# Optimization experiments

Measured on AMD Instinct MI355X. Metric: run time of the kernel, lower is better.

The kernel has to match this reference:

```python
import jax, jax.numpy as jnp
import numpy as np

IN_DIMS = 4
DEPTH = 4
C = IN_DIMS + 1                     # channels after time augmentation
SIG = sum(C ** k for k in range(1, DEPTH + 1))  # 780
N, T = 64, 1024


def setup_inputs() -> dict:
    key = jax.random.key(0)
    k1, k2, k3, k4, k5 = jax.random.split(key, 5)
    batch = jax.random.normal(k1, (N, T, IN_DIMS), dtype=jnp.float32)
    s_c = 1.0 / np.sqrt(C)
    conv_w = jax.random.normal(k2, (C, C), dtype=jnp.float32) * s_c
    conv_b = jax.random.normal(k3, (C,), dtype=jnp.float32) * s_c
    s_l = 1.0 / np.sqrt(SIG)
    lin_w = jax.random.normal(k4, (SIG, SIG), dtype=jnp.float32) * s_l
    lin_b = jax.random.normal(k5, (SIG,), dtype=jnp.float32) * s_l
    return {"batch": batch, "conv_w": conv_w, "conv_b": conv_b,
            "lin_w": lin_w, "lin_b": lin_b}


def _stream_signature(path):
    """Streamed path signature with zero basepoint.

    path: (n, t, C). Returns (n, t, SIG) where entry t is the signature of
    the piecewise-linear path (0, path[0], ..., path[t]) truncated at DEPTH,
    levels flattened in lexicographic (row-major) order like signatory.
    """
    n = path.shape[0]
    # increments; basepoint=True means first increment is path[:,0] - 0
    dx = jnp.concatenate([path[:, :1, :], path[:, 1:, :] - path[:, :-1, :]], axis=1)
    init = tuple(jnp.zeros((n, C ** k), path.dtype) for k in range(1, DEPTH + 1))

    def step(levels, d):
        # exp(d) in the truncated tensor algebra: e_k = d^{(x)k} / k!
        e = [d]
        for k in range(2, DEPTH + 1):
            e.append((jnp.einsum('na,nb->nab', e[-1], d) / k).reshape(n, -1))
        # Chen: new_k = e_k + S_k + sum_{i=1}^{k-1} S_i (x) e_{k-i}
        new = []
        for k in range(1, DEPTH + 1):
            acc = levels[k - 1] + e[k - 1]
            for i in range(1, k):
                acc = acc + jnp.einsum('na,nb->nab', levels[i - 1], e[k - i - 1]).reshape(n, -1)
            new.append(acc)
        new = tuple(new)
        return new, jnp.concatenate(new, axis=-1)

    _, ys = jax.lax.scan(step, init, jnp.swapaxes(dx, 0, 1))  # ys: (t, n, SIG)
    return jnp.swapaxes(ys, 0, 1)


def reference(batch, conv_w, conv_b, lin_w, lin_b):
    n, t, _ = batch.shape
    # time augmentation: append channel arange(1,T+1)/T
    time = (jnp.arange(1, t + 1, dtype=batch.dtype) / t)[None, :, None]
    a = jnp.concatenate([batch, jnp.broadcast_to(time, (n, t, 1))], axis=-1)  # (n,t,C)
    # kernel-size-1 conv1d == pointwise linear over channels
    b = a @ conv_w.T + conv_b                                                  # (n,t,C)
    c = _stream_signature(b)                                                   # (n,t,SIG)
    # zero out the first stream entry (torch.concat of zeros with c[:,1:,:])
    c = jnp.concatenate([jnp.zeros((n, 1, SIG), c.dtype), c[:, 1:, :]], axis=1)
    return jnp.tanh(c @ lin_w.T + lin_b)
```

## Files before the change

### kernel.cpp

```cpp
#include <hip/hip_runtime.h>
#include <math.h>

#define N_B 64
#define T_LEN 1024
#define IN_D 4
#define CH 5
#define SIG 780
#define KP 800
#define SEG_LEN 16
#define N_SEG 64
#define SC_L1 1.0f
#define SC_L2 0.25f
#define SC_L3 0.0625f
#define SC_L4 0.015625f

typedef _Float16 f16x8 __attribute__((ext_vector_type(8)));
typedef float f32x4 __attribute__((ext_vector_type(4)));

typedef __attribute__((address_space(1))) const void* as1cp;
typedef __attribute__((address_space(3))) void* as3p;

#define VMCNT(n) asm volatile("s_waitcnt vmcnt(" #n ")" ::: "memory")

__device__ __forceinline__ float fast_tanh(float x) {
  float ax = fabsf(x);
  float e = __expf(-2.0f * ax);
  float r = (1.0f - e) * __builtin_amdgcn_rcpf(1.0f + e);
  return copysignf(r, x);
}

__global__ __launch_bounds__(256) void conv_kernel(
    const float* __restrict__ batch,
    const float* __restrict__ conv_w,
    const float* __restrict__ conv_b,
    float* __restrict__ b_out) {
  int idx = blockIdx.x * blockDim.x + threadIdx.x;
  if (idx >= N_B * T_LEN) return;
  int t = idx & (T_LEN - 1);
  const float* a = batch + (size_t)idx * IN_D;
  float a0 = a[0], a1 = a[1], a2 = a[2], a3 = a[3];
  float tm = (float)(t + 1) / (float)T_LEN;
  float* o = b_out + (size_t)idx * CH;
#pragma unroll
  for (int j = 0; j < CH; ++j) {
    const float* w = conv_w + j * CH;
    float r = conv_b[j];
    r = fmaf(tm, w[4], r);
    r = fmaf(a3, w[3], r);
    r = fmaf(a2, w[2], r);
    r = fmaf(a1, w[1], r);
    r = fmaf(a0, w[0], r);
    o[j] = r;
  }
}

__global__ __launch_bounds__(320) void seg_kernel(
    const float* __restrict__ batch,
    const float* __restrict__ conv_w,
    const float* __restrict__ conv_b,
    float* __restrict__ P) {
  int s = blockIdx.x;
  int n = blockIdx.y;
  int tid = threadIdx.x;

  __shared__ float S[2][SIG];
  __shared__ float bc[(SEG_LEN + 1) * CH];
  __shared__ float dsh[SEG_LEN][CH];

  for (int i = tid; i < SIG; i += 320) S[0][i] = 0.0f;
  if (tid < (SEG_LEN + 1) * CH) {
    int r = s * SEG_LEN - 1 + tid / CH, ch = tid % CH;
    float v = 0.0f;
    if (r >= 0) {
      const float* a = batch + ((size_t)n * T_LEN + r) * IN_D;
      const float* w = conv_w + ch * CH;
      v = conv_b[ch];
      v = fmaf(a[0], w[0], v);
      v = fmaf(a[1], w[1], v);
      v = fmaf(a[2], w[2], v);
      v = fmaf(a[3], w[3], v);
      v = fmaf((float)(r + 1) * (1.0f / T_LEN), w[4], v);
    }
    bc[tid] = v;
  }
  __syncthreads();
  if (tid < SEG_LEN * CH) {
    int j = tid / CH, ch = tid % CH;
    dsh[j][ch] = bc[(j + 1) * CH + ch] - bc[j * CH + ch];
  }

  const int x0 = tid;
  const int x1 = tid + 320;
  const bool has1 = (tid < 305);
  const int a0i = x0 / 125, b0i = (x0 / 25) % 5, c0i = (x0 / 5) % 5, d0i = x0 % 5;
  const int a1i = x1 / 125, b1i = (x1 / 25) % 5, c1i = (x1 / 5) % 5, d1i = x1 % 5;
  const int s2_0 = x0 / 25, s3_0 = x0 / 5;
  const int s2_1 = x1 / 25, s3_1 = x1 / 5;
  const bool hasL3 = (tid < 125);
  const int ya = tid / 25, yb = (tid / 5) % 5, yc = tid % 5;
  const bool hasL2 = (tid < 25);
  const int za = tid / 5, zb = tid % 5;
  const bool hasL1 = (tid < CH);
  __syncthreads();

  int c = 0;
  for (int j = 0; j < SEG_LEN; ++j) {
    const float* Sc = S[c];
    float* Sn = S[c ^ 1];
    float n4_0, n4_1 = 0.0f, n3 = 0.0f, n2 = 0.0f, n1 = 0.0f;
    {
      float tH = fmaf(0.25f, dsh[j][a0i], Sc[a0i]);
      tH = fmaf((1.0f / 3.0f) * dsh[j][b0i], tH, Sc[5 + s2_0]);
      tH = fmaf(0.5f * dsh[j][c0i], tH, Sc[30 + s3_0]);
      n4_0 = fmaf(dsh[j][d0i], tH, Sc[155 + x0]);
    }
    if (has1) {
      float tH = fmaf(0.25f, dsh[j][a1i], Sc[a1i]);
      tH = fmaf((1.0f / 3.0f) * dsh[j][b1i], tH, Sc[5 + s2_1]);
      tH = fmaf(0.5f * dsh[j][c1i], tH, Sc[30 + s3_1]);
      n4_1 = fmaf(dsh[j][d1i], tH, Sc[155 + x1]);
    }
    if (hasL3) {
      float tH = fmaf((1.0f / 3.0f), dsh[j][ya], Sc[ya]);
      tH = fmaf(0.5f * dsh[j][yb], tH, Sc[5 + ya * 5 + yb]);
      n3 = fmaf(dsh[j][yc], tH, Sc[30 + tid]);
    }
    if (hasL2) {
      float tH = fmaf(0.5f, dsh[j][za], Sc[za]);
      n2 = fmaf(dsh[j][zb], tH, Sc[5 + tid]);
    }
    if (hasL1) n1 = Sc[tid] + dsh[j][tid];
    Sn[155 + x0] = n4_0;
    if (has1) Sn[155 + x1] = n4_1;
    if (hasL3) Sn[30 + tid] = n3;
    if (hasL2) Sn[5 + tid] = n2;
    if (hasL1) Sn[tid] = n1;
    __syncthreads();
    c ^= 1;
  }

  float* Pr = P + ((size_t)n * N_SEG + s) * SIG;
  for (int i = tid; i < SIG; i += 320) Pr[i] = S[c][i];
}

__global__ __launch_bounds__(640) void prefix_kernel(float* __restrict__ P) {
  int n = blockIdx.x;
  int tid = threadIdx.x;
  __shared__ float A[2][SIG];
  __shared__ float Bs[SIG];

  float* Pn = P + (size_t)n * N_SEG * SIG;
  for (int i = tid; i < SIG; i += 640) A[0][i] = Pn[i];
  int i0 = tid, i1 = tid + 640;
  float r0 = 0.f, r1 = 0.f;
  if (i0 < SIG) r0 = Pn[SIG + i0];
  if (i1 < SIG) r1 = Pn[SIG + i1];

  const int e4 = tid;
  const int q4a = e4 / 125, r125 = e4 % 125, r25 = e4 % 25, r5 = e4 % 5;
  const int e4d5 = e4 / 5, e4d25 = e4 / 25;
  const int e3 = tid;
  const int e3a = e3 / 25, e3r25 = e3 % 25, e3r5 = e3 % 5, e3d5 = e3 / 5;
  const int e2 = tid - 125;
  const int e1 = tid - 150;

  int c = 0;
  for (int s = 1; s < N_SEG; ++s) {
    if (i0 < SIG) Bs[i0] = r0;
    if (i1 < SIG) Bs[i1] = r1;
    __syncthreads();
    if (s + 1 < N_SEG) {
      const float* Pnx = Pn + (size_t)(s + 1) * SIG;
      if (i0 < SIG) r0 = Pnx[i0];
      if (i1 < SIG) r1 = Pnx[i1];
    }
    const float* Ac = A[c];
    float* An = A[c ^ 1];
    float* Po = Pn + (size_t)s * SIG;
    if (tid < 625) {
      float v4 = Ac[155 + e4] + Bs[155 + e4];
      v4 = fmaf(Ac[30 + e4d5], Bs[r5], v4);
      v4 = fmaf(Ac[5 + e4d25], Bs[5 + r25], v4);
      v4 = fmaf(Ac[q4a], Bs[30 + r125], v4);
      An[155 + e4] = v4; Po[155 + e4] = v4;
    }
    if (tid < 125) {
      float v3 = Ac[30 + e3] + Bs[30 + e3];
      v3 = fmaf(Ac[5 + e3d5], Bs[e3r5], v3);
      v3 = fmaf(Ac[e3a], Bs[5 + e3r25], v3);
      An[30 + e3] = v3; Po[30 + e3] = v3;
    } else if (tid < 150) {
      float v2 = Ac[5 + e2] + Bs[5 + e2];
      v2 = fmaf(Ac[e2 / 5], Bs[e2 % 5], v2);
      An[5 + e2] = v2; Po[5 + e2] = v2;
    } else if (tid < 155) {
      float v1 = Ac[e1] + Bs[e1];
      An[e1] = v1; Po[e1] = v1;
    }
    c ^= 1;
  }
}

__global__ __launch_bounds__(320) void emit_kernel(
    const float* __restrict__ batch,
    const float* __restrict__ conv_w,
    const float* __restrict__ conv_b,
    const float* __restrict__ P,
    _Float16* __restrict__ c1,
    _Float16* __restrict__ c2) {
  int s = blockIdx.x;
  int n = blockIdx.y;
  int tid = threadIdx.x;

  __shared__ float S[2][SIG];
  __shared__ float bc[(SEG_LEN + 1) * CH];
  __shared__ float dsh[SEG_LEN][CH];
  __shared__ __align__(16) _Float16 row1[2][KP];
  __shared__ __align__(16) _Float16 row2[2][KP];

  if (s == 0) {
    for (int i = tid; i < SIG; i += 320) S[0][i] = 0.0f;
  } else {
    const float* Pr = P + ((size_t)n * N_SEG + (s - 1)) * SIG;
    for (int i = tid; i < SIG; i += 320) S[0][i] = Pr[i];
  }
  if (tid < (SEG_LEN + 1) * CH) {
    int r = s * SEG_LEN - 1 + tid / CH, ch = tid % CH;
    float v = 0.0f;
    if (r >= 0) {
      const float* a = batch + ((size_t)n * T_LEN + r) * IN_D;
      const float* w = conv_w + ch * CH;
      v = conv_b[ch];
      v = fmaf(a[0], w[0], v);
      v = fmaf(a[1], w[1], v);
      v = fmaf(a[2], w[2], v);
      v = fmaf(a[3], w[3], v);
      v = fmaf((float)(r + 1) * (1.0f / T_LEN), w[4], v);
    }
    bc[tid] = v;
  }
  if (tid < KP - SIG) {
    row1[0][SIG + tid] = (_Float16)0.0f;
    row1[1][SIG + tid] = (_Float16)0.0f;
    row2[0][SIG + tid] = (_Float16)0.0f;
    row2[1][SIG + tid] = (_Float16)0.0f;
  }
  __syncthreads();
  if (tid < SEG_LEN * CH) {
    int j = tid / CH, ch = tid % CH;
    dsh[j][ch] = bc[(j + 1) * CH + ch] - bc[j * CH + ch];
  }

  const int x0 = tid;
  const int x1 = tid + 320;
  const bool has1 = (tid < 305);
  const int a0i = x0 / 125, b0i = (x0 / 25) % 5, c0i = (x0 / 5) % 5, d0i = x0 % 5;
  const int a1i = x1 / 125, b1i = (x1 / 25) % 5, c1i = (x1 / 5) % 5, d1i = x1 % 5;
  const int s2_0 = x0 / 25, s3_0 = x0 / 5;
  const int s2_1 = x1 / 25, s3_1 = x1 / 5;
  const bool hasL3 = (tid < 125);
  const int ya = tid / 25, yb = (tid / 5) % 5, yc = tid % 5;
  const bool hasL2 = (tid < 25);
  const int za = tid / 5, zb = tid % 5;
  const bool hasL1 = (tid < CH);
  __syncthreads();

  int c = 0;
  for (int j = 0; j < SEG_LEN; ++j) {
    int t = s * SEG_LEN + j;
    const float* Sc = S[c];
    float* Sn = S[c ^ 1];
    float n4_0, n4_1 = 0.0f, n3 = 0.0f, n2 = 0.0f, n1 = 0.0f;
    {
      float tH = fmaf(0.25f, dsh[j][a0i], Sc[a0i]);
      tH = fmaf((1.0f / 3.0f) * dsh[j][b0i], tH, Sc[5 + s2_0]);
      tH = fmaf(0.5f * dsh[j][c0i], tH, Sc[30 + s3_0]);
      n4_0 = fmaf(dsh[j][d0i], tH, Sc[155 + x0]);
    }
    if (has1) {
      float tH = fmaf(0.25f, dsh[j][a1i], Sc[a1i]);
      tH = fmaf((1.0f / 3.0f) * dsh[j][b1i], tH, Sc[5 + s2_1]);
      tH = fmaf(0.5f * dsh[j][c1i], tH, Sc[30 + s3_1]);
      n4_1 = fmaf(dsh[j][d1i], tH, Sc[155 + x1]);
    }
    if (hasL3) {
      float tH = fmaf((1.0f / 3.0f), dsh[j][ya], Sc[ya]);
      tH = fmaf(0.5f * dsh[j][yb], tH, Sc[5 + ya * 5 + yb]);
      n3 = fmaf(dsh[j][yc], tH, Sc[30 + tid]);
    }
    if (hasL2) {
      float tH = fmaf(0.5f, dsh[j][za], Sc[za]);
      n2 = fmaf(dsh[j][zb], tH, Sc[5 + tid]);
    }
    if (hasL1) n1 = Sc[tid] + dsh[j][tid];

    if (j > 0) {
      size_t base = ((size_t)n * T_LEN + (t - 1)) * KP;
      if (tid < 100) {
        *(float4*)(c1 + base + tid * 8) = *(const float4*)&row1[c][tid * 8];
      } else if (tid < 200) {
        int cc = tid - 100;
        *(float4*)(c2 + base + cc * 8) = *(const float4*)&row2[c][cc * 8];
      }
    }

    Sn[155 + x0] = n4_0;
    if (has1) Sn[155 + x1] = n4_1;
    if (hasL3) Sn[30 + tid] = n3;
    if (hasL2) Sn[5 + tid] = n2;
    if (hasL1) Sn[tid] = n1;

    float z = (t == 0) ? 0.0f : 1.0f;
    {
      float v = n4_0 * SC_L4 * z;
      _Float16 h = (_Float16)v;
      row1[c ^ 1][155 + x0] = h; row2[c ^ 1][155 + x0] = (_Float16)(v - (float)h);
    }
    if (has1) {
      float v = n4_1 * SC_L4 * z;
      _Float16 h = (_Float16)v;
      row1[c ^ 1][155 + x1] = h; row2[c ^ 1][155 + x1] = (_Float16)(v - (float)h);
    }
    if (hasL3) {
      float v = n3 * SC_L3 * z;
      _Float16 h = (_Float16)v;
      row1[c ^ 1][30 + tid] = h; row2[c ^ 1][30 + tid] = (_Float16)(v - (float)h);
    }
    if (hasL2) {
      float v = n2 * SC_L2 * z;
      _Float16 h = (_Float16)v;
      row1[c ^ 1][5 + tid] = h; row2[c ^ 1][5 + tid] = (_Float16)(v - (float)h);
    }
    if (hasL1) {
      float v = n1 * SC_L1 * z;
      _Float16 h = (_Float16)v;
      row1[c ^ 1][tid] = h; row2[c ^ 1][tid] = (_Float16)(v - (float)h);
    }
    __syncthreads();
    c ^= 1;
  }
  {
    size_t base = ((size_t)n * T_LEN + (s * SEG_LEN + SEG_LEN - 1)) * KP;
    if (tid < 100) {
      *(float4*)(c1 + base + tid * 8) = *(const float4*)&row1[c][tid * 8];
    } else if (tid < 200) {
      int cc = tid - 100;
      *(float4*)(c2 + base + cc * 8) = *(const float4*)&row2[c][cc * 8];
    }
  }
}

__global__ __launch_bounds__(256) void wconv_kernel(
    const float* __restrict__ W,
    _Float16* __restrict__ w1,
    _Float16* __restrict__ w2) {
  int idx = blockIdx.x * blockDim.x + threadIdx.x;
  if (idx >= 896 * KP) return;
  int nn = idx / KP, k = idx % KP;
  float v = 0.0f;
  if (nn < SIG && k < SIG) {
    float sc = (k < 5) ? 1.0f : (k < 30) ? 4.0f : (k < 155) ? 16.0f : 64.0f;
    v = W[(size_t)nn * SIG + k] * sc;
  }
  _Float16 h = (_Float16)v;
  w1[idx] = h;
  w2[idx] = (_Float16)(v - (float)h);
}

__global__ __launch_bounds__(512, 2) void gemm_mfma(
    const _Float16* __restrict__ A1p, const _Float16* __restrict__ A2p,
    const _Float16* __restrict__ B1p, const _Float16* __restrict__ B2p,
    const float* __restrict__ bias, float* __restrict__ out) {
  __shared__ _Float16 Al[3][2][256 * 32];
  __shared__ _Float16 Bl[3][2][128 * 32];

  int tid = threadIdx.x;
  int lane = tid & 63, wid = tid >> 6;
  int wm = wid >> 1, wn = wid & 1;

  int b = blockIdx.x;
  int xcd = b & 7, sidx = b >> 3;
  int mt = (sidx / 7) * 8 + xcd;
  int nt = sidx % 7;
  int m0 = mt * 256;
  int n0 = nt * 128;

  f32x4 acc[4][4];
#pragma unroll
  for (int i = 0; i < 4; ++i)
#pragma unroll
    for (int j = 0; j < 4; ++j) acc[i][j] = (f32x4){0.f, 0.f, 0.f, 0.f};

  int sr = lane >> 2, scn = lane & 3;
  int swst = (sr ^ (sr >> 2)) & 3;
  int qg = scn ^ swst;
  int fr = lane & 15, fq = lane >> 4;
  int swf = (fr ^ (fr >> 2)) & 3;
  int fchunk = fq ^ swf;

  auto stageA = [&](int kb, int buf, int i) {
    int k0 = kb * 32;
    int linear = wid * 4 + i;
    int plane = linear >> 4, grp = linear & 15;
    size_t g = (size_t)(m0 + grp * 16 + sr) * KP + k0 + qg * 8;
    const _Float16* src = (plane ? A2p : A1p) + g;
    __builtin_amdgcn_global_load_lds((as1cp)src, (as3p)(&Al[buf][plane][grp * 512]), 16, 0, 0);
  };
  auto stageB = [&](int kb, int buf, int i) {
    int k0 = kb * 32;
    int linear = wid * 2 + i;
    int plane = linear >> 3, grp = linear & 7;
    size_t g = (size_t)(n0 + grp * 16 + sr) * KP + k0 + qg * 8;
    const _Float16* src = (plane ? B2p : B1p) + g;
    __builtin_amdgcn_global_load_lds((as1cp)src, (as3p)(&Bl[buf][plane][grp * 512]), 16, 0, 0);
  };

#pragma unroll
  for (int i = 0; i < 4; ++i) stageA(0, 0, i);
#pragma unroll
  for (int i = 0; i < 2; ++i) stageB(0, 0, i);
#pragma unroll
  for (int i = 0; i < 4; ++i) stageA(1, 1, i);
#pragma unroll
  for (int i = 0; i < 2; ++i) stageB(1, 1, i);

  f16x8 b1f[4], b2f[4];
  int cur = 0;
#pragma unroll 1
  for (int kb = 0; kb < 25; ++kb) {
    int nx = cur + 2; if (nx >= 3) nx -= 3;
    bool pf = (kb + 2 < 25);
    if (kb < 24) { VMCNT(6); } else { VMCNT(0); }
    __builtin_amdgcn_s_barrier();
    __builtin_amdgcn_sched_barrier(0);
#pragma unroll
    for (int ph = 0; ph < 2; ++ph) {
      f16x8 a1f[2], a2f[2];
      if (ph == 0) {
#pragma unroll
        for (int tn = 0; tn < 4; ++tn) {
          int off = (wn * 64 + tn * 16 + fr) * 32 + fchunk * 8;
          b1f[tn] = *(const f16x8*)&Bl[cur][0][off];
          b2f[tn] = *(const f16x8*)&Bl[cur][1][off];
        }
      }
#pragma unroll
      for (int t = 0; t < 2; ++t) {
        int tm = ph * 2 + t;
        int off = (wm * 64 + tm * 16 + fr) * 32 + fchunk * 8;
        a1f[t] = *(const f16x8*)&Al[cur][0][off];
        a2f[t] = *(const f16x8*)&Al[cur][1][off];
      }
      if (pf) {
        stageA(kb + 2, nx, ph * 2 + 0);
        stageA(kb + 2, nx, ph * 2 + 1);
        stageB(kb + 2, nx, ph);
      }
      __builtin_amdgcn_s_barrier();
      __builtin_amdgcn_sched_barrier(0);
      __builtin_amdgcn_s_setprio(1);
#pragma unroll
      for (int t = 0; t < 2; ++t) {
        int tm = ph * 2 + t;
#pragma unroll
        for (int tn = 0; tn < 4; ++tn) {
          acc[tm][tn] = __builtin_amdgcn_mfma_f32_16x16x32_f16(a1f[t], b1f[tn], acc[tm][tn], 0, 0, 0);
          acc[tm][tn] = __builtin_amdgcn_mfma_f32_16x16x32_f16(a1f[t], b2f[tn], acc[tm][tn], 0, 0, 0);
          acc[tm][tn] = __builtin_amdgcn_mfma_f32_16x16x32_f16(a2f[t], b1f[tn], acc[tm][tn], 0, 0, 0);
        }
      }
      __builtin_amdgcn_s_setprio(0);
    }
    cur = cur + 1; if (cur >= 3) cur -= 3;
  }
  __syncthreads();

  float* ep = (float*)(&Al[0][0][0]) + wid * 2112;

  float bv[4];
#pragma unroll
  for (int tn = 0; tn < 4; ++tn) {
    int nn = n0 + wn * 64 + tn * 16 + fr;
    bv[tn] = (nn < SIG) ? bias[nn] : 0.0f;
  }
#pragma unroll
  for (int h = 0; h < 2; ++h) {
#pragma unroll
    for (int tm2 = 0; tm2 < 2; ++tm2) {
      int tm = h * 2 + tm2;
#pragma unroll
      for (int tn = 0; tn < 4; ++tn) {
#pragma unroll
        for (int r = 0; r < 4; ++r) {
          int lr = tm2 * 16 + fq * 4 + r;
          int lc = tn * 16 + fr;
          ep[lr * 66 + lc] = fast_tanh(acc[tm][tn][r] + bv[tn]);
        }
      }
    }
#pragma unroll
    for (int p = 0; p < 2; ++p) {
      int lr = lane & 31;
      int ck = (lane >> 5) * 2 + p;
      int gm = m0 + wm * 64 + h * 32 + lr;
      int gc0 = n0 + wn * 64 + ck * 16;
#pragma unroll
      for (int q = 0; q < 4; ++q) {
        int col = gc0 + q * 4;
        if (col + 3 < SIG) {
          *(float4*)(out + (size_t)gm * SIG + col) =
              *(const float4*)&ep[lr * 66 + ck * 16 + q * 4];
        } else if (col < SIG) {
#pragma unroll
          for (int e = 0; e < 4; ++e) {
            int c2 = col + e;
            if (c2 < SIG) out[(size_t)gm * SIG + c2] = ep[lr * 66 + ck * 16 + q * 4 + e];
          }
        }
      }
    }
  }
}

__global__ __launch_bounds__(320) void sig_kernel_fb(
    const float* __restrict__ b_in, float* __restrict__ c_out) {
  int n = blockIdx.x;
  int tid = threadIdx.x;
  __shared__ float S[SIG];
  __shared__ float bc[64 * CH];
  __shared__ float dsh[CH];
  __shared__ float pb[CH];
  for (int i = tid; i < SIG; i += 320) S[i] = 0.0f;
  if (tid < CH) pb[tid] = 0.0f;
  const float* bn = b_in + (size_t)n * T_LEN * CH;
  float* cn = c_out + (size_t)n * T_LEN * SIG;
  const int x0 = tid, x1 = tid + 320;
  const bool has1 = (tid < 305);
  const int a0i = x0 / 125, b0i = (x0 / 25) % 5, c0i = (x0 / 5) % 5, d0i = x0 % 5;
  const int a1i = x1 / 125, b1i = (x1 / 25) % 5, c1i = (x1 / 5) % 5, d1i = x1 % 5;
  const int s2_0 = x0 / 25, s3_0 = x0 / 5, s2_1 = x1 / 25, s3_1 = x1 / 5;
  const bool hasL3 = (tid < 125);
  const int ya = tid / 25, yb = (tid / 5) % 5, yc = tid % 5;
  const bool hasL2 = (tid < 25);
  const int za = tid / 5, zb = tid % 5;
  const bool hasL1 = (tid < CH);
  for (int t = 0; t < T_LEN; ++t) {
    if ((t & 63) == 0) {
      __syncthreads();
      bc[tid] = bn[t * CH + tid];
      __syncthreads();
    }
    if (tid < CH) {
      float cur = bc[(t & 63) * CH + tid];
      dsh[tid] = cur - pb[tid];
      pb[tid] = cur;
    }
    __syncthreads();
    float n4_0, n4_1 = 0.0f, n3 = 0.0f, n2 = 0.0f, n1 = 0.0f;
    {
      float tH = fmaf(0.25f, dsh[a0i], S[a0i]);
      tH = fmaf((1.0f / 3.0f) * dsh[b0i], tH, S[5 + s2_0]);
      tH = fmaf(0.5f * dsh[c0i], tH, S[30 + s3_0]);
      n4_0 = fmaf(dsh[d0i], tH, S[155 + x0]);
    }
    if (has1) {
      float tH = fmaf(0.25f, dsh[a1i], S[a1i]);
      tH = fmaf((1.0f / 3.0f) * dsh[b1i], tH, S[5 + s2_1]);
      tH = fmaf(0.5f * dsh[c1i], tH, S[30 + s3_1]);
      n4_1 = fmaf(dsh[d1i], tH, S[155 + x1]);
    }
    if (hasL3) {
      float tH = fmaf((1.0f / 3.0f), dsh[ya], S[ya]);
      tH = fmaf(0.5f * dsh[yb], tH, S[5 + ya * 5 + yb]);
      n3 = fmaf(dsh[yc], tH, S[30 + tid]);
    }
    if (hasL2) {
      float tH = fmaf(0.5f, dsh[za], S[za]);
      n2 = fmaf(dsh[zb], tH, S[5 + tid]);
    }
    if (hasL1) n1 = S[tid] + dsh[tid];
    __syncthreads();
    S[155 + x0] = n4_0;
    if (has1) S[155 + x1] = n4_1;
    if (hasL3) S[30 + tid] = n3;
    if (hasL2) S[5 + tid] = n2;
    if (hasL1) S[tid] = n1;
    float* crow = cn + (size_t)t * SIG;
    float z = (t == 0) ? 0.0f : 1.0f;
    crow[155 + x0] = n4_0 * z;
    if (has1) crow[155 + x1] = n4_1 * z;
    if (hasL3) crow[30 + tid] = n3 * z;
    if (hasL2) crow[5 + tid] = n2 * z;
    if (hasL1) crow[tid] = n1 * z;
    __syncthreads();
  }
}

#define BM 256
#define BN 64
#define BK 16
__global__ __launch_bounds__(256) void gemm_tanh_fb(
    const float* __restrict__ Cmat, const float* __restrict__ W,
    const float* __restrict__ bias, float* __restrict__ out) {
  __shared__ float As[BK][BM + 4];
  __shared__ float Ws[BK][BN + 4];
  int tid = threadIdx.x;
  int tx = tid & 7, ty = tid >> 3;
  int m0 = blockIdx.x * BM, n0 = blockIdx.y * BN;
  float acc[8][8];
#pragma unroll
  for (int i = 0; i < 8; ++i)
#pragma unroll
    for (int j = 0; j < 8; ++j) acc[i][j] = 0.0f;
  for (int kb = 0; kb < SIG; kb += BK) {
    __syncthreads();
#pragma unroll
    for (int p = 0; p < 4; ++p) {
      int id = tid + p * 256;
      int row = id >> 2, kg = (id & 3) * 4, gk = kb + kg;
      float4 v = make_float4(0.f, 0.f, 0.f, 0.f);
      if (gk < SIG) v = *(const float4*)(Cmat + (size_t)(m0 + row) * SIG + gk);
      As[kg + 0][row] = v.x; As[kg + 1][row] = v.y;
      As[kg + 2][row] = v.z; As[kg + 3][row] = v.w;
    }
    {
      int row = tid >> 2, kg = (tid & 3) * 4, gk = kb + kg, wr = n0 + row;
      float4 v = make_float4(0.f, 0.f, 0.f, 0.f);
      if (gk < SIG && wr < SIG) v = *(const float4*)(W + (size_t)wr * SIG + gk);
      Ws[kg + 0][row] = v.x; Ws[kg + 1][row] = v.y;
      Ws[kg + 2][row] = v.z; Ws[kg + 3][row] = v.w;
    }
    __syncthreads();
#pragma unroll
    for (int k = 0; k < BK; ++k) {
      float af[8], wf[8];
      *(float4*)&af[0] = *(const float4*)&As[k][ty * 8];
      *(float4*)&af[4] = *(const float4*)&As[k][ty * 8 + 4];
      *(float4*)&wf[0] = *(const float4*)&Ws[k][tx * 8];
      *(float4*)&wf[4] = *(const float4*)&Ws[k][tx * 8 + 4];
#pragma unroll
      for (int i = 0; i < 8; ++i)
#pragma unroll
        for (int j = 0; j < 8; ++j) acc[i][j] = fmaf(af[i], wf[j], acc[i][j]);
    }
  }
#pragma unroll
  for (int i = 0; i < 8; ++i) {
    int m = m0 + ty * 8 + i;
    float* orow = out + (size_t)m * SIG;
#pragma unroll
    for (int jj = 0; jj < 8; jj += 4) {
      int col = n0 + tx * 8 + jj;
      if (col < SIG) {
        float4 r;
        r.x = tanhf(acc[i][jj + 0] + bias[col + 0]);
        r.y = tanhf(acc[i][jj + 1] + bias[col + 1]);
        r.z = tanhf(acc[i][jj + 2] + bias[col + 2]);
        r.w = tanhf(acc[i][jj + 3] + bias[col + 3]);
        *(float4*)(orow + col) = r;
      }
    }
  }
}

extern "C" void kernel_launch(void* const* d_in, const int* in_sizes, int n_in,
                              void* d_out, int out_size, void* d_ws, size_t ws_size,
                              hipStream_t stream) {
  const float* batch = (const float*)d_in[0];
  const float* conv_w = (const float*)d_in[1];
  const float* conv_b = (const float*)d_in[2];
  const float* lin_w = (const float*)d_in[3];
  const float* lin_b = (const float*)d_in[4];
  float* out = (float*)d_out;

  const size_t plane_elems = (size_t)N_B * T_LEN * KP;
  const size_t wplane_elems = (size_t)896 * KP;
  const size_t P_elems = (size_t)N_B * N_SEG * SIG;
  const size_t bp_elems = (size_t)N_B * T_LEN * CH;
  const size_t need_big = 2 * plane_elems * sizeof(_Float16) +
                          2 * wplane_elems * sizeof(_Float16) +
                          P_elems * sizeof(float);

  if (ws_size >= need_big) {
    _Float16* c1 = (_Float16*)d_ws;
    _Float16* c2 = c1 + plane_elems;
    _Float16* w1 = c2 + plane_elems;
    _Float16* w2 = w1 + wplane_elems;
    float* P = (float*)(w2 + wplane_elems);

    wconv_kernel<<<dim3((896 * KP + 255) / 256), dim3(256), 0, stream>>>(
        lin_w, w1, w2);
    seg_kernel<<<dim3(N_SEG, N_B), dim3(320), 0, stream>>>(batch, conv_w, conv_b, P);
    prefix_kernel<<<dim3(N_B), dim3(640), 0, stream>>>(P);
    emit_kernel<<<dim3(N_SEG, N_B), dim3(320), 0, stream>>>(
        batch, conv_w, conv_b, P, c1, c2);
    gemm_mfma<<<dim3(1792), dim3(512), 0, stream>>>(c1, c2, w1, w2, lin_b, out);
  } else {
    float* b_path = (float*)d_ws;
    float* c_sig = (float*)d_ws + bp_elems;
    conv_kernel<<<dim3((N_B * T_LEN + 255) / 256), dim3(256), 0, stream>>>(
        batch, conv_w, conv_b, b_path);
    sig_kernel_fb<<<dim3(N_B), dim3(320), 0, stream>>>(b_path, c_sig);
    gemm_tanh_fb<<<dim3((N_B * T_LEN) / BM, (SIG + BN - 1) / BN), dim3(256), 0, stream>>>(
        c_sig, lin_w, lin_b, out);
  }
}
```

Before: 658.7 us.

## Shrink GEMM tile to 128x64 with more blocks and higher occupancy

```diff
diff --git a/kernel.cpp b/kernel.cpp
--- a/kernel.cpp
+++ b/kernel.cpp
@@ -367,29 +367,27 @@
   w2[idx] = (_Float16)(v - (float)h);
 }
 
-__global__ __launch_bounds__(512, 2) void gemm_mfma(
+__global__ __launch_bounds__(512, 4) void gemm_mfma(
     const _Float16* __restrict__ A1p, const _Float16* __restrict__ A2p,
     const _Float16* __restrict__ B1p, const _Float16* __restrict__ B2p,
     const float* __restrict__ bias, float* __restrict__ out) {
-  __shared__ _Float16 Al[3][2][256 * 32];
-  __shared__ _Float16 Bl[3][2][128 * 32];
+  __shared__ _Float16 Al[3][2][128 * 32];
+  __shared__ _Float16 Bl[3][2][64 * 32];
 
   int tid = threadIdx.x;
   int lane = tid & 63, wid = tid >> 6;
-  int wm = wid >> 1, wn = wid & 1;
+  int wm = wid >> 2, wn = wid & 3;
 
   int b = blockIdx.x;
   int xcd = b & 7, sidx = b >> 3;
-  int mt = (sidx / 7) * 8 + xcd;
-  int nt = sidx % 7;
-  int m0 = mt * 256;
-  int n0 = nt * 128;
-
-  f32x4 acc[4][4];
-#pragma unroll
-  for (int i = 0; i < 4; ++i)
-#pragma unroll
-    for (int j = 0; j < 4; ++j) acc[i][j] = (f32x4){0.f, 0.f, 0.f, 0.f};
+  int mt = (sidx / 14) * 8 + xcd;
+  int nt = sidx % 14;
+  int m0 = mt * 128;
+  int n0 = nt * 64;
+
+  f32x4 acc[4];
+#pragma unroll
+  for (int i = 0; i < 4; ++i) acc[i] = (f32x4){0.f, 0.f, 0.f, 0.f};
 
   int sr = lane >> 2, scn = lane & 3;
   int swst = (sr ^ (sr >> 2)) & 3;
@@ -400,125 +398,103 @@
 
   auto stageA = [&](int kb, int buf, int i) {
     int k0 = kb * 32;
-    int linear = wid * 4 + i;
-    int plane = linear >> 4, grp = linear & 15;
+    int linear = wid * 2 + i;
+    int plane = linear >> 3, grp = linear & 7;
     size_t g = (size_t)(m0 + grp * 16 + sr) * KP + k0 + qg * 8;
     const _Float16* src = (plane ? A2p : A1p) + g;
     __builtin_amdgcn_global_load_lds((as1cp)src, (as3p)(&Al[buf][plane][grp * 512]), 16, 0, 0);
   };
-  auto stageB = [&](int kb, int buf, int i) {
+  auto stageB = [&](int kb, int buf) {
     int k0 = kb * 32;
-    int linear = wid * 2 + i;
-    int plane = linear >> 3, grp = linear & 7;
+    int plane = wid >> 2, grp = wid & 3;
     size_t g = (size_t)(n0 + grp * 16 + sr) * KP + k0 + qg * 8;
     const _Float16* src = (plane ? B2p : B1p) + g;
     __builtin_amdgcn_global_load_lds((as1cp)src, (as3p)(&Bl[buf][plane][grp * 512]), 16, 0, 0);
   };
 
 #pragma unroll
-  for (int i = 0; i < 4; ++i) stageA(0, 0, i);
-#pragma unroll
-  for (int i = 0; i < 2; ++i) stageB(0, 0, i);
-#pragma unroll
-  for (int i = 0; i < 4; ++i) stageA(1, 1, i);
-#pragma unroll
-  for (int i = 0; i < 2; ++i) stageB(1, 1, i);
-
-  f16x8 b1f[4], b2f[4];
+  for (int i = 0; i < 2; ++i) stageA(0, 0, i);
+  stageB(0, 0);
+#pragma unroll
+  for (int i = 0; i < 2; ++i) stageA(1, 1, i);
+  stageB(1, 1);
+
   int cur = 0;
 #pragma unroll 1
   for (int kb = 0; kb < 25; ++kb) {
     int nx = cur + 2; if (nx >= 3) nx -= 3;
     bool pf = (kb + 2 < 25);
-    if (kb < 24) { VMCNT(6); } else { VMCNT(0); }
+    if (kb < 24) { VMCNT(3); } else { VMCNT(0); }
     __builtin_amdgcn_s_barrier();
     __builtin_amdgcn_sched_barrier(0);
-#pragma unroll
-    for (int ph = 0; ph < 2; ++ph) {
-      f16x8 a1f[2], a2f[2];
-      if (ph == 0) {
-#pragma unroll
-        for (int tn = 0; tn < 4; ++tn) {
-          int off = (wn * 64 + tn * 16 + fr) * 32 + fchunk * 8;
-          b1f[tn] = *(const f16x8*)&Bl[cur][0][off];
-          b2f[tn] = *(const f16x8*)&Bl[cur][1][off];
+    f16x8 a1f[4], a2f[4], b1f, b2f;
+#pragma unroll
+    for (int tm = 0; tm < 4; ++tm) {
+      int off = (wm * 64 + tm * 16 + fr) * 32 + fchunk * 8;
+      a1f[tm] = *(const f16x8*)&Al[cur][0][off];
+      a2f[tm] = *(const f16x8*)&Al[cur][1][off];
+    }
+    {
+      int off = (wn * 16 + fr) * 32 + fchunk * 8;
+      b1f = *(const f16x8*)&Bl[cur][0][off];
+      b2f = *(const f16x8*)&Bl[cur][1][off];
+    }
+    if (pf) {
+      stageA(kb + 2, nx, 0);
+      stageA(kb + 2, nx, 1);
+      stageB(kb + 2, nx);
+    }
+    __builtin_amdgcn_s_barrier();
+    __builtin_amdgcn_sched_barrier(0);
+    __builtin_amdgcn_s_setprio(1);
+#pragma unroll
+    for (int tm = 0; tm < 4; ++tm) {
+      acc[tm] = __builtin_amdgcn_mfma_f32_16x16x32_f16(a1f[tm], b1f, acc[tm], 0, 0, 0);
+      acc[tm] = __builtin_amdgcn_mfma_f32_16x16x32_f16(a1f[tm], b2f, acc[tm], 0, 0, 0);
+      acc[tm] = __builtin_amdgcn_mfma_f32_16x16x32_f16(a2f[tm], b1f, acc[tm], 0, 0, 0);
+    }
+    __builtin_amdgcn_s_setprio(0);
+    cur = cur + 1; if (cur >= 3) cur -= 3;
+  }
+  __syncthreads();
+
+  float* ep = (float*)(&Al[0][0][0]) + wid * 640;
+
+  float bv;
+  {
+    int nn = n0 + wn * 16 + fr;
+    bv = (nn < SIG) ? bias[nn] : 0.0f;
+  }
+#pragma unroll
+  for (int h = 0; h < 2; ++h) {
+#pragma unroll
+    for (int tm2 = 0; tm2 < 2; ++tm2) {
+      int tm = h * 2 + tm2;
+#pragma unroll
+      for (int r = 0; r < 4; ++r) {
+        int lr = tm2 * 16 + fq * 4 + r;
+        ep[lr * 20 + fr] = fast_tanh(acc[tm][r] + bv);
+      }
+    }
+    __builtin_amdgcn_sched_barrier(0);
+#pragma unroll
+    for (int q = 0; q < 2; ++q) {
+      int lr = lane & 31;
+      int c0 = (lane >> 5) * 8 + q * 4;
+      int gm = m0 + wm * 64 + h * 32 + lr;
+      int col = n0 + wn * 16 + c0;
+      if (col + 3 < SIG) {
+        *(float4*)(out + (size_t)gm * SIG + col) =
+            *(const float4*)&ep[lr * 20 + c0];
+      } else if (col < SIG) {
+#pragma unroll
+        for (int e = 0; e < 4; ++e) {
+          int c2 = col + e;
+          if (c2 < SIG) out[(size_t)gm * SIG + c2] = ep[lr * 20 + c0 + e];
         }
       }
-#pragma unroll
-      for (int t = 0; t < 2; ++t) {
-        int tm = ph * 2 + t;
-        int off = (wm * 64 + tm * 16 + fr) * 32 + fchunk * 8;
-        a1f[t] = *(const f16x8*)&Al[cur][0][off];
-        a2f[t] = *(const f16x8*)&Al[cur][1][off];
-      }
-      if (pf) {
-        stageA(kb + 2, nx, ph * 2 + 0);
-        stageA(kb + 2, nx, ph * 2 + 1);
-        stageB(kb + 2, nx, ph);
-      }
-      __builtin_amdgcn_s_barrier();
-      __builtin_amdgcn_sched_barrier(0);
-      __builtin_amdgcn_s_setprio(1);
-#pragma unroll
-      for (int t = 0; t < 2; ++t) {
-        int tm = ph * 2 + t;
-#pragma unroll
-        for (int tn = 0; tn < 4; ++tn) {
-          acc[tm][tn] = __builtin_amdgcn_mfma_f32_16x16x32_f16(a1f[t], b1f[tn], acc[tm][tn], 0, 0, 0);
-          acc[tm][tn] = __builtin_amdgcn_mfma_f32_16x16x32_f16(a1f[t], b2f[tn], acc[tm][tn], 0, 0, 0);
-          acc[tm][tn] = __builtin_amdgcn_mfma_f32_16x16x32_f16(a2f[t], b1f[tn], acc[tm][tn], 0, 0, 0);
-        }
-      }
-      __builtin_amdgcn_s_setprio(0);
-    }
-    cur = cur + 1; if (cur >= 3) cur -= 3;
-  }
-  __syncthreads();
-
-  float* ep = (float*)(&Al[0][0][0]) + wid * 2112;
-
-  float bv[4];
-#pragma unroll
-  for (int tn = 0; tn < 4; ++tn) {
-    int nn = n0 + wn * 64 + tn * 16 + fr;
-    bv[tn] = (nn < SIG) ? bias[nn] : 0.0f;
-  }
-#pragma unroll
-  for (int h = 0; h < 2; ++h) {
-#pragma unroll
-    for (int tm2 = 0; tm2 < 2; ++tm2) {
-      int tm = h * 2 + tm2;
-#pragma unroll
-      for (int tn = 0; tn < 4; ++tn) {
-#pragma unroll
-        for (int r = 0; r < 4; ++r) {
-          int lr = tm2 * 16 + fq * 4 + r;
-          int lc = tn * 16 + fr;
-          ep[lr * 66 + lc] = fast_tanh(acc[tm][tn][r] + bv[tn]);
-        }
-      }
-    }
-#pragma unroll
-    for (int p = 0; p < 2; ++p) {
-      int lr = lane & 31;
-      int ck = (lane >> 5) * 2 + p;
-      int gm = m0 + wm * 64 + h * 32 + lr;
-      int gc0 = n0 + wn * 64 + ck * 16;
-#pragma unroll
-      for (int q = 0; q < 4; ++q) {
-        int col = gc0 + q * 4;
-        if (col + 3 < SIG) {
-          *(float4*)(out + (size_t)gm * SIG + col) =
-              *(const float4*)&ep[lr * 66 + ck * 16 + q * 4];
-        } else if (col < SIG) {
-#pragma unroll
-          for (int e = 0; e < 4; ++e) {
-            int c2 = col + e;
-            if (c2 < SIG) out[(size_t)gm * SIG + c2] = ep[lr * 66 + ck * 16 + q * 4 + e];
-          }
-        }
-      }
-    }
+    }
+    __builtin_amdgcn_sched_barrier(0);
   }
 }
 
@@ -694,7 +670,7 @@
     prefix_kernel<<<dim3(N_B), dim3(640), 0, stream>>>(P);
     emit_kernel<<<dim3(N_SEG, N_B), dim3(320), 0, stream>>>(
         batch, conv_w, conv_b, P, c1, c2);
-    gemm_mfma<<<dim3(1792), dim3(512), 0, stream>>>(c1, c2, w1, w2, lin_b, out);
+    gemm_mfma<<<dim3(7168), dim3(512), 0, stream>>>(c1, c2, w1, w2, lin_b, out);
   } else {
     float* b_path = (float*)d_ws;
     float* c_sig = (float*)d_ws + bp_elems;
```

Result: slower. 728.1 us (+10.5%).
